# Kernel optimization log

Hardware: AMD Instinct MI355X
Metric: run time of the kernel (lower is better)

## Reference

```python
import jax, jax.numpy as jnp
import numpy as np
import math

B, H, L, N2 = 16, 256, 4096, 32  # batch, d_model, seq len, d_state//2


def setup_inputs() -> dict:
    key = jax.random.key(0)
    ks = jax.random.split(key, 7)
    u = jax.random.normal(ks[0], (B, H, L), dtype=jnp.float32)
    # torch init: rand(H) * (log(dt_max) - log(dt_min)) + log(dt_min)
    log_dt = jax.random.uniform(ks[1], (H,), dtype=jnp.float32,
                                minval=math.log(1e-3), maxval=math.log(1e-1))
    C_real = jax.random.normal(ks[2], (H, N2), dtype=jnp.float32)
    C_imag = jax.random.normal(ks[3], (H, N2), dtype=jnp.float32)
    log_A_real = jnp.full((H, N2), math.log(0.5), dtype=jnp.float32)
    A_imag = jnp.array(jnp.broadcast_to(math.pi * jnp.arange(N2, dtype=jnp.float32), (H, N2)))
    D = jax.random.normal(ks[4], (H,), dtype=jnp.float32)
    W_out = jax.random.normal(ks[5], (2 * H, H), dtype=jnp.float32) / math.sqrt(H)
    b_out = jax.random.normal(ks[6], (2 * H,), dtype=jnp.float32) * 0.01
    return dict(u=u, log_dt=log_dt, C_real=C_real, C_imag=C_imag,
                log_A_real=log_A_real, A_imag=A_imag, D=D, W_out=W_out, b_out=b_out)


def _s4d_kernel(log_dt, C_real, C_imag, log_A_real, A_imag, length):
    dt = jnp.exp(log_dt)                             # (H,)
    A = -jnp.exp(log_A_real) + 1j * A_imag           # (H, N2) complex
    dtA = A * dt[:, None]                            # (H, N2)
    C = (C_real + 1j * C_imag) * (jnp.exp(dtA) - 1.0) / A
    # Vandermonde: exp(dtA * l) for l in [0, L)
    V = jnp.exp(dtA[:, :, None] * jnp.arange(length, dtype=jnp.float32))  # (H, N2, L)
    return 2.0 * jnp.einsum('hn,hnl->hl', C, V).real  # (H, L)


def reference(u, log_dt, C_real, C_imag, log_A_real, A_imag, D, W_out, b_out):
    length = u.shape[-1]
    k = _s4d_kernel(log_dt, C_real, C_imag, log_A_real, A_imag, length)
    # FFT-based causal long convolution (zero-padded to 2L)
    n = 2 * length
    y = jnp.fft.irfft(jnp.fft.rfft(u, n=n) * jnp.fft.rfft(k, n=n), n=n)[..., :length]
    y = y + u * D[:, None]
    y = jax.nn.gelu(y, approximate=False)            # eval mode: dropout is identity
    # 1x1 Conv1d (h -> 2h) followed by GLU over the channel dim
    z = jnp.einsum('oh,bhl->bol', W_out, y) + b_out[:, None]  # (B, 2H, L)
    a, b = jnp.split(z, 2, axis=-2)
    return a * jax.nn.sigmoid(b)                     # (B, H, L)
```

## Files before the change

### kernel.cpp

```cpp
#include <hip/hip_runtime.h>

#define NB 16
#define NH 256
#define NL 4096
#define NN 32

typedef short s8v __attribute__((ext_vector_type(8)));
typedef float f4v __attribute__((ext_vector_type(4)));
typedef unsigned short u8h __attribute__((ext_vector_type(8)));

__device__ __forceinline__ unsigned short f2bf(float x) {
    unsigned int u = __float_as_uint(x);
    unsigned int r = u + 0x7FFFu + ((u >> 16) & 1u);
    return (unsigned short)(r >> 16);
}
__device__ __forceinline__ float bf2f(unsigned short b) {
    return __uint_as_float(((unsigned int)b) << 16);
}
__device__ __forceinline__ unsigned int cvt_pk_bf16(float lo, float hi) {
    unsigned int r;
    asm("v_cvt_pk_bf16_f32 %0, %1, %2" : "=v"(r) : "v"(lo), "v"(hi));
    return r;
}

__global__ __launch_bounds__(64) void precompute_kernel(
        const float* __restrict__ log_dt,
        const float* __restrict__ Cr,
        const float* __restrict__ Ci,
        const float* __restrict__ lar,
        const float* __restrict__ aim,
        const float* __restrict__ Dvec,
        float* __restrict__ w32c,
        unsigned short* __restrict__ Mp,
        unsigned short* __restrict__ Em,
        unsigned short* __restrict__ Tm,
        const float* __restrict__ W,
        unsigned short* __restrict__ Wbf) {
    const int h = blockIdx.x;
    const int tid = threadIdx.x;
    __shared__ float sRe[32][33];
    __shared__ float sTd[32];
    __shared__ unsigned short sMp[64 * 32];
    __shared__ unsigned short sEm[32 * 64];

    if (tid < 32) {
        const int n = tid;
        const int idx = h * 32 + n;
        float dt = expf(log_dt[h]);
        float ar = -expf(lar[idx]);
        float ai = aim[idx];
        float dar = ar * dt, dai = ai * dt;
        float er = expf(dar);
        float wr = er * cosf(dai), wi = er * sinf(dai);
        float Er = wr - 1.0f, Ei = wi;
        float den = ar * ar + ai * ai;
        float fr = (Er * ar + Ei * ai) / den;
        float fi = (Ei * ar - Er * ai) / den;
        float cr = Cr[idx], ci = Ci[idx];
        float c2r = 2.0f * (cr * fr - ci * fi);
        float c2i = 2.0f * (cr * fi + ci * fr);
        float e32 = expf(32.0f * dar);
        w32c[h * 64 + 2 * n]     = e32 * cosf(32.0f * dai);
        w32c[h * 64 + 2 * n + 1] = e32 * sinf(32.0f * dai);
        float pr = 1.0f, pi = 0.0f;
        for (int e = 0; e < 32; ++e) {
            sMp[(2 * n) * 32 + (31 - e)]     = f2bf(pr);
            sMp[(2 * n + 1) * 32 + (31 - e)] = f2bf(pi);
            float npr = pr * wr - pi * wi;
            pi = fmaf(pr, wi, pi * wr);
            pr = npr;
        }
        float gr = c2r, gi = c2i;
        for (int e = 0; e <= 32; ++e) {
            if (e < 32) sRe[e][n] = gr;
            if (e >= 1) {
                sEm[(e - 1) * 64 + 2 * n]     = f2bf(gr);
                sEm[(e - 1) * 64 + 2 * n + 1] = f2bf(-gi);
            }
            float ngr = gr * wr - gi * wi;
            gi = fmaf(gr, wi, gi * wr);
            gr = ngr;
        }
    }
    __syncthreads();
    if (tid < 32) {
        float a = 0.0f;
        #pragma unroll
        for (int n = 0; n < 32; ++n) a += sRe[tid][n];
        sTd[tid] = a;
    }
    __syncthreads();
    const float dh = Dvec[h];
    unsigned short* tmh = Tm + h * 1024;
    for (int i = 0; i < 16; ++i) {
        int idx = tid * 16 + i;
        int j = idx >> 5, tt = idx & 31;
        float v = (j >= tt) ? sTd[j - tt] : 0.0f;
        if (j == tt) v += dh;
        tmh[idx] = f2bf(v);
    }
    uint4* mp4 = (uint4*)(Mp + h * 2048);
    uint4* em4 = (uint4*)(Em + h * 2048);
    const uint4* smp4 = (const uint4*)sMp;
    const uint4* sem4 = (const uint4*)sEm;
    #pragma unroll
    for (int k = 0; k < 4; ++k) {
        mp4[k * 64 + tid] = smp4[k * 64 + tid];
        em4[k * 64 + tid] = sem4[k * 64 + tid];
    }
    const int gidx = h * 64 + tid;
    #pragma unroll
    for (int k = 0; k < 2; ++k) {
        int i = gidx + k * (NH * 64);
        float4 v = ((const float4*)W)[i];
        ushort4 o;
        o.x = f2bf(v.x); o.y = f2bf(v.y); o.z = f2bf(v.z); o.w = f2bf(v.w);
        ((ushort4*)Wbf)[i] = o;
    }
}

__global__ __launch_bounds__(256) void scan_mfma_kernel(
        const float* __restrict__ u,
        const float* __restrict__ w32c,
        const unsigned short* __restrict__ Mp,
        const unsigned short* __restrict__ Tm,
        const unsigned short* __restrict__ Em,
        unsigned short* __restrict__ ybf) {
    const int bh = blockIdx.x;
    const int h = bh & (NH - 1);
    const int tid = threadIdx.x;
    const int lane = tid & 63;
    const int wv = tid >> 6;
    const int g = lane >> 4, c = lane & 15;

    __shared__ float ldsT[256];
    __shared__ __align__(16) unsigned int ldsP[128 * 36];

    s8v bu[2];
    #pragma unroll
    for (int ntl = 0; ntl < 2; ++ntl) {
        const float* usrc = u + (size_t)bh * NL + (((2 * wv + ntl) * 16 + c) << 5) + g * 8;
        float4 x0 = *(const float4*)usrc;
        float4 x1 = *(const float4*)(usrc + 4);
        union { unsigned int w[4]; s8v v; } cv;
        cv.w[0] = cvt_pk_bf16(x0.x, x0.y);
        cv.w[1] = cvt_pk_bf16(x0.z, x0.w);
        cv.w[2] = cvt_pk_bf16(x1.x, x1.y);
        cv.w[3] = cvt_pk_bf16(x1.z, x1.w);
        bu[ntl] = cv.v;
    }

    const unsigned short* mph = Mp + h * 2048;
    f4v p1[4][2];
    #pragma unroll
    for (int mt = 0; mt < 4; ++mt) {
        s8v am = *(const s8v*)(mph + (mt * 16 + c) * 32 + g * 8);
        p1[mt][0] = (f4v){0.f,0.f,0.f,0.f};
        p1[mt][1] = (f4v){0.f,0.f,0.f,0.f};
        p1[mt][0] = __builtin_amdgcn_mfma_f32_16x16x32_bf16(am, bu[0], p1[mt][0], 0,0,0);
        p1[mt][1] = __builtin_amdgcn_mfma_f32_16x16x32_bf16(am, bu[1], p1[mt][1], 0,0,0);
    }
    #pragma unroll
    for (int mt = 0; mt < 4; ++mt)
        #pragma unroll
        for (int ntl = 0; ntl < 2; ++ntl) {
            const int chunk = (2 * wv + ntl) * 16 + c;
            f4v v = p1[mt][ntl];
            unsigned int lo = cvt_pk_bf16(v[0], v[1]);
            unsigned int hi = cvt_pk_bf16(v[2], v[3]);
            *(uint2*)&ldsP[chunk * 36 + mt * 8 + 2 * g] = make_uint2(lo, hi);
        }
    __syncthreads();

    float wr_b = 0.f, wi_b = 0.f;
    if (tid < 128) {
        const int n = tid & 31, seg = tid >> 5;
        wr_b = w32c[h * 64 + 2 * n];
        wi_b = w32c[h * 64 + 2 * n + 1];
        float sr = 0.f, si = 0.f;
        const int base = seg * 32;
        for (int t = 0; t < 32; ++t) {
            const int chunk = base + t;
            unsigned int pv = ldsP[chunk * 36 + n];
            ldsP[chunk * 36 + n] = cvt_pk_bf16(sr, si);
            float Pr = bf2f((unsigned short)(pv & 0xFFFF));
            float Pi = bf2f((unsigned short)(pv >> 16));
            float nsr = fmaf(wr_b, sr, fmaf(-wi_b, si, Pr));
            float nsi = fmaf(wr_b, si, fmaf(wi_b, sr, Pi));
            sr = nsr; si = nsi;
        }
        *(float2*)&ldsT[(seg * 32 + n) * 2] = make_float2(sr, si);
    }
    __syncthreads();
    if (tid < 128) {
        const int n = tid & 31, seg = tid >> 5;
        if (seg > 0) {
            float qr = wr_b, qi = wi_b;
            #pragma unroll
            for (int sq = 0; sq < 5; ++sq) {
                float nr = qr * qr - qi * qi;
                float ni = 2.0f * qr * qi;
                qr = nr; qi = ni;
            }
            float Qr = 0.f, Qi = 0.f;
            #pragma unroll
            for (int sp = 0; sp < 3; ++sp) {
                float2 Tv = *(const float2*)&ldsT[(sp * 32 + n) * 2];
                if (sp < seg) {
                    float nQr = fmaf(qr, Qr, fmaf(-qi, Qi, Tv.x));
                    float nQi = fmaf(qr, Qi, fmaf(qi, Qr, Tv.y));
                    Qr = nQr; Qi = nQi;
                }
            }
            float gr = Qr, gi = Qi;
            const int base = seg * 32;
            for (int t = 0; t < 32; ++t) {
                const int chunk = base + t;
                unsigned int sv = ldsP[chunk * 36 + n];
                float fr2 = bf2f((unsigned short)(sv & 0xFFFF)) + gr;
                float fi2 = bf2f((unsigned short)(sv >> 16)) + gi;
                ldsP[chunk * 36 + n] = cvt_pk_bf16(fr2, fi2);
                float ngr = wr_b * gr - wi_b * gi;
                float ngi = fmaf(wr_b, gi, wi_b * gr);
                gr = ngr; gi = ngi;
            }
        }
    }
    __syncthreads();

    const unsigned short* tmh = Tm + h * 1024;
    const unsigned short* emh = Em + h * 2048;
    const unsigned short* sbase = (const unsigned short*)ldsP;
    f4v a2[2][2];
    #pragma unroll
    for (int mt = 0; mt < 2; ++mt) {
        a2[mt][0] = (f4v){0.f,0.f,0.f,0.f};
        a2[mt][1] = (f4v){0.f,0.f,0.f,0.f};
        s8v at = *(const s8v*)(tmh + (mt * 16 + c) * 32 + g * 8);
        a2[mt][0] = __builtin_amdgcn_mfma_f32_16x16x32_bf16(at, bu[0], a2[mt][0], 0,0,0);
        a2[mt][1] = __builtin_amdgcn_mfma_f32_16x16x32_bf16(at, bu[1], a2[mt][1], 0,0,0);
    }
    #pragma unroll
    for (int ksub = 0; ksub < 2; ++ksub) {
        s8v bs[2];
        #pragma unroll
        for (int ntl = 0; ntl < 2; ++ntl) {
            const int chunk = (2 * wv + ntl) * 16 + c;
            bs[ntl] = *(const s8v*)(sbase + chunk * 72 + ksub * 32 + g * 8);
        }
        #pragma unroll
        for (int mt = 0; mt < 2; ++mt) {
            s8v ae = *(const s8v*)(emh + (mt * 16 + c) * 64 + ksub * 32 + g * 8);
            a2[mt][0] = __builtin_amdgcn_mfma_f32_16x16x32_bf16(ae, bs[0], a2[mt][0], 0,0,0);
            a2[mt][1] = __builtin_amdgcn_mfma_f32_16x16x32_bf16(ae, bs[1], a2[mt][1], 0,0,0);
        }
    }

    unsigned short* yrow = ybf + (size_t)bh * NL;
    #pragma unroll
    for (int mt = 0; mt < 2; ++mt)
        #pragma unroll
        for (int ntl = 0; ntl < 2; ++ntl) {
            const int chunk = (2 * wv + ntl) * 16 + c;
            f4v v = a2[mt][ntl];
            float gv[4];
            #pragma unroll
            for (int r = 0; r < 4; ++r) {
                float x = v[r];
                gv[r] = 0.5f * x * (1.0f + erff(x * 0.70710678118654752f));
            }
            unsigned int lo = cvt_pk_bf16(gv[0], gv[1]);
            unsigned int hi = cvt_pk_bf16(gv[2], gv[3]);
            *(uint2*)(yrow + chunk * 32 + mt * 16 + 4 * g) = make_uint2(lo, hi);
        }
}

__global__ __launch_bounds__(512) void gemm_glu_mfma(
        const unsigned short* __restrict__ ybf,
        const unsigned short* __restrict__ Wbf,
        const float* __restrict__ bo,
        float* __restrict__ out) {
    const int l0 = blockIdx.x * 64;
    const int b  = blockIdx.y;
    const int tid = threadIdx.x;
    const int lane = tid & 63;
    const int wv = tid >> 6;
    const int g = lane >> 4, c = lane & 15;

    __shared__ __align__(16) unsigned int ldsY[64 * 132];

    {
        const int r  = tid >> 1;
        const int hh = tid & 1;
        const int kp = r >> 1, hb = r & 1;
        const int kps = kp ^ (hh << 4);
        const unsigned short* ysrc = ybf + ((size_t)b * NH + r) * NL + l0 + hh * 32;
        uint4 v0 = ((const uint4*)ysrc)[0];
        uint4 v1 = ((const uint4*)ysrc)[1];
        uint4 v2 = ((const uint4*)ysrc)[2];
        uint4 v3 = ((const uint4*)ysrc)[3];
        unsigned short* lds16 = (unsigned short*)ldsY;
        const int base16 = ((hh * 32) * 132 + kps) * 2 + hb;
        u8h a0 = *(const u8h*)&v0, a1 = *(const u8h*)&v1;
        u8h a2 = *(const u8h*)&v2, a3 = *(const u8h*)&v3;
        #pragma unroll
        for (int j = 0; j < 8; ++j) {
            lds16[base16 + (j)      * 264] = a0[j];
            lds16[base16 + (j + 8)  * 264] = a1[j];
            lds16[base16 + (j + 16) * 264] = a2[j];
            lds16[base16 + (j + 24) * 264] = a3[j];
        }
    }
    __syncthreads();

    f4v acc[4][4];
    #pragma unroll
    for (int m = 0; m < 4; ++m)
        #pragma unroll
        for (int n = 0; n < 4; ++n)
            acc[m][n] = (f4v){0.f, 0.f, 0.f, 0.f};

    int wrow[4];
    wrow[0] = wv * 32 + c;
    wrow[1] = wrow[0] + 16;
    wrow[2] = wrow[0] + 256;
    wrow[3] = wrow[1] + 256;

    s8v afr[4];
    #pragma unroll
    for (int m = 0; m < 4; ++m)
        afr[m] = *(const s8v*)(Wbf + wrow[m] * NH + g * 8);

    #pragma unroll
    for (int ks = 0; ks < 8; ++ks) {
        s8v acur[4];
        #pragma unroll
        for (int m = 0; m < 4; ++m) acur[m] = afr[m];
        if (ks < 7) {
            #pragma unroll
            for (int m = 0; m < 4; ++m)
                afr[m] = *(const s8v*)(Wbf + wrow[m] * NH + (ks + 1) * 32 + g * 8);
        }
        s8v bfr[4];
        #pragma unroll
        for (int n = 0; n < 4; ++n) {
            const int colb = (ks * 16 + g * 4) ^ ((n >> 1) << 4);
            bfr[n] = *(const s8v*)&ldsY[(n * 16 + c) * 132 + colb];
        }
        #pragma unroll
        for (int m = 0; m < 4; ++m)
            #pragma unroll
            for (int n = 0; n < 4; ++n)
                acc[m][n] = __builtin_amdgcn_mfma_f32_16x16x32_bf16(
                    acur[m], bfr[n], acc[m][n], 0, 0, 0);
    }

    #pragma unroll
    for (int m = 0; m < 2; ++m) {
        const int o0 = wv * 32 + m * 16 + g * 4;
        float4 ba = *(const float4*)(bo + o0);
        float4 bb = *(const float4*)(bo + NH + o0);
        const float baj[4] = {ba.x, ba.y, ba.z, ba.w};
        const float bbj[4] = {bb.x, bb.y, bb.z, bb.w};
        #pragma unroll
        for (int j = 0; j < 4; ++j) {
            float* orow = out + ((size_t)(b * NH + o0 + j)) * NL + l0 + c;
            #pragma unroll
            for (int n = 0; n < 4; ++n) {
                float za = acc[m][n][j] + baj[j];
                float zb = acc[m + 2][n][j] + bbj[j];
                float s = __builtin_amdgcn_rcpf(1.0f + __expf(-zb));
                orow[n * 16] = za * s;
            }
        }
    }
}

extern "C" void kernel_launch(void* const* d_in, const int* in_sizes, int n_in,
                              void* d_out, int out_size, void* d_ws, size_t ws_size,
                              hipStream_t stream) {
    (void)in_sizes; (void)n_in; (void)out_size; (void)ws_size;
    const float* u      = (const float*)d_in[0];
    const float* log_dt = (const float*)d_in[1];
    const float* Cr     = (const float*)d_in[2];
    const float* Ci     = (const float*)d_in[3];
    const float* lar    = (const float*)d_in[4];
    const float* aim    = (const float*)d_in[5];
    const float* Dvec   = (const float*)d_in[6];
    const float* W      = (const float*)d_in[7];
    const float* bo     = (const float*)d_in[8];
    float* out = (float*)d_out;

    char* ws = (char*)d_ws;
    float*          w32c = (float*)ws;
    unsigned short* Mp   = (unsigned short*)(ws + 65536);
    unsigned short* Em   = (unsigned short*)(ws + 1114112);
    unsigned short* Tm   = (unsigned short*)(ws + 2162688);
    unsigned short* Wbf  = (unsigned short*)(ws + 2686976);
    unsigned short* ybf  = (unsigned short*)(ws + 2949120);

    precompute_kernel<<<dim3(NH), dim3(64), 0, stream>>>(
        log_dt, Cr, Ci, lar, aim, Dvec, w32c, Mp, Em, Tm, W, Wbf);
    scan_mfma_kernel<<<dim3(NB * NH), dim3(256), 0, stream>>>(u, w32c, Mp, Tm, Em, ybf);
    gemm_glu_mfma<<<dim3(NL / 64, NB), dim3(512), 0, stream>>>(ybf, Wbf, bo, out);
}
```

Before: 93.89 us.

## Use all 256 threads for chunk scan and pack bf16 pairs in LDS staging

```diff
diff --git a/kernel.cpp b/kernel.cpp
--- a/kernel.cpp
+++ b/kernel.cpp
@@ -133,7 +133,7 @@
     const int wv = tid >> 6;
     const int g = lane >> 4, c = lane & 15;
 
-    __shared__ float ldsT[256];
+    __shared__ float ldsT[512];
     __shared__ __align__(16) unsigned int ldsP[128 * 36];
 
     s8v bu[2];
@@ -172,14 +172,13 @@
         }
     __syncthreads();
 
-    float wr_b = 0.f, wi_b = 0.f;
-    if (tid < 128) {
+    {
         const int n = tid & 31, seg = tid >> 5;
-        wr_b = w32c[h * 64 + 2 * n];
-        wi_b = w32c[h * 64 + 2 * n + 1];
+        const float wr_b = w32c[h * 64 + 2 * n];
+        const float wi_b = w32c[h * 64 + 2 * n + 1];
         float sr = 0.f, si = 0.f;
-        const int base = seg * 32;
-        for (int t = 0; t < 32; ++t) {
+        const int base = seg * 16;
+        for (int t = 0; t < 16; ++t) {
             const int chunk = base + t;
             unsigned int pv = ldsP[chunk * 36 + n];
             ldsP[chunk * 36 + n] = cvt_pk_bf16(sr, si);
@@ -190,21 +189,18 @@
             sr = nsr; si = nsi;
         }
         *(float2*)&ldsT[(seg * 32 + n) * 2] = make_float2(sr, si);
-    }
-    __syncthreads();
-    if (tid < 128) {
-        const int n = tid & 31, seg = tid >> 5;
+        __syncthreads();
         if (seg > 0) {
             float qr = wr_b, qi = wi_b;
             #pragma unroll
-            for (int sq = 0; sq < 5; ++sq) {
+            for (int sq = 0; sq < 4; ++sq) {
                 float nr = qr * qr - qi * qi;
                 float ni = 2.0f * qr * qi;
                 qr = nr; qi = ni;
             }
             float Qr = 0.f, Qi = 0.f;
             #pragma unroll
-            for (int sp = 0; sp < 3; ++sp) {
+            for (int sp = 0; sp < 7; ++sp) {
                 float2 Tv = *(const float2*)&ldsT[(sp * 32 + n) * 2];
                 if (sp < seg) {
                     float nQr = fmaf(qr, Qr, fmaf(-qi, Qi, Tv.x));
@@ -213,8 +209,7 @@
                 }
             }
             float gr = Qr, gi = Qi;
-            const int base = seg * 32;
-            for (int t = 0; t < 32; ++t) {
+            for (int t = 0; t < 16; ++t) {
                 const int chunk = base + t;
                 unsigned int sv = ldsP[chunk * 36 + n];
                 float fr2 = bf2f((unsigned short)(sv & 0xFFFF)) + gr;
@@ -290,25 +285,24 @@
     __shared__ __align__(16) unsigned int ldsY[64 * 132];
 
     {
-        const int r  = tid >> 1;
-        const int hh = tid & 1;
-        const int kp = r >> 1, hb = r & 1;
-        const int kps = kp ^ (hh << 4);
-        const unsigned short* ysrc = ybf + ((size_t)b * NH + r) * NL + l0 + hh * 32;
-        uint4 v0 = ((const uint4*)ysrc)[0];
-        uint4 v1 = ((const uint4*)ysrc)[1];
-        uint4 v2 = ((const uint4*)ysrc)[2];
-        uint4 v3 = ((const uint4*)ysrc)[3];
-        unsigned short* lds16 = (unsigned short*)ldsY;
-        const int base16 = ((hh * 32) * 132 + kps) * 2 + hb;
-        u8h a0 = *(const u8h*)&v0, a1 = *(const u8h*)&v1;
-        u8h a2 = *(const u8h*)&v2, a3 = *(const u8h*)&v3;
+        const int kp = tid >> 2;
+        const int lq = tid & 3;
+        const int kps = kp ^ ((lq >> 1) << 4);
+        const unsigned short* ysrcA = ybf + ((size_t)b * NH + 2 * kp) * NL + l0 + lq * 16;
+        const unsigned short* ysrcB = ysrcA + NL;
+        uint4 a0 = ((const uint4*)ysrcA)[0];
+        uint4 a1 = ((const uint4*)ysrcA)[1];
+        uint4 b0 = ((const uint4*)ysrcB)[0];
+        uint4 b1 = ((const uint4*)ysrcB)[1];
+        u8h ah0 = *(const u8h*)&a0, ah1 = *(const u8h*)&a1;
+        u8h bh0 = *(const u8h*)&b0, bh1 = *(const u8h*)&b1;
+        const int lbase = lq * 16;
         #pragma unroll
         for (int j = 0; j < 8; ++j) {
-            lds16[base16 + (j)      * 264] = a0[j];
-            lds16[base16 + (j + 8)  * 264] = a1[j];
-            lds16[base16 + (j + 16) * 264] = a2[j];
-            lds16[base16 + (j + 24) * 264] = a3[j];
+            ldsY[(lbase + j) * 132 + kps] =
+                (unsigned int)ah0[j] | ((unsigned int)bh0[j] << 16);
+            ldsY[(lbase + j + 8) * 132 + kps] =
+                (unsigned int)ah1[j] | ((unsigned int)bh1[j] << 16);
         }
     }
     __syncthreads();
```

After: 87.69 us. 1.07x faster.
